# Kernel tuning notes

Measured on AMD Instinct MI355X. Metric: run time of the kernel, lower is better.

The kernel has to match this reference:

```python
import jax, jax.numpy as jnp
import numpy as np

HIDDEN = 1280
HEADS = 16
HEAD_DIM = HIDDEN // HEADS  # 80
B, N = 2, 2048


def _rotate_half(x):
    half = x.shape[-1] // 2
    return jnp.concatenate([-x[..., half:], x[..., :half]], axis=-1)


def setup_inputs() -> dict:
    key = jax.random.key(0)
    ks = jax.random.split(key, 7)
    x = jax.random.normal(ks[0], (B, N, HIDDEN), dtype=jnp.float32)
    cos = jax.random.uniform(ks[1], (N, HEAD_DIM), dtype=jnp.float32)
    sin = jax.random.uniform(ks[2], (N, HEAD_DIM), dtype=jnp.float32)
    s = 1.0 / np.sqrt(HIDDEN)
    qkv_w = jax.random.normal(ks[3], (HIDDEN, 3 * HIDDEN), dtype=jnp.float32) * s
    qkv_b = jax.random.normal(ks[4], (3 * HIDDEN,), dtype=jnp.float32) * 0.02
    proj_w = jax.random.normal(ks[5], (HIDDEN, HIDDEN), dtype=jnp.float32) * s
    proj_b = jax.random.normal(ks[6], (HIDDEN,), dtype=jnp.float32) * 0.02
    return {"x": x, "cos": cos, "sin": sin, "qkv_w": qkv_w, "qkv_b": qkv_b,
            "proj_w": proj_w, "proj_b": proj_b}


def reference(x, cos, sin, qkv_w, qkv_b, proj_w, proj_b):
    b, n, _ = x.shape
    scale = 1.0 / np.sqrt(HEAD_DIM).astype(np.float32)
    # fused QKV projection
    qkv = x @ qkv_w + qkv_b                                # [b, n, 3*hidden]
    qkv = qkv.reshape(b, n, 3, HEADS, HEAD_DIM)
    qkv = jnp.transpose(qkv, (2, 0, 3, 1, 4))              # [3, b, h, n, hd]
    q, k, v = qkv[0], qkv[1], qkv[2]
    # 2D RoPE
    cos_b = cos[None, None, :, :]
    sin_b = sin[None, None, :, :]
    q = q * cos_b + _rotate_half(q) * sin_b
    k = k * cos_b + _rotate_half(k) * sin_b
    # manual softmax attention
    scores = jnp.einsum('bhqd,bhkd->bhqk', q, k) * scale   # [b, h, n, n]
    attn = jax.nn.softmax(scores, axis=-1)
    out = jnp.einsum('bhqk,bhkd->bhqd', attn, v)           # [b, h, n, hd]
    out = jnp.transpose(out, (0, 2, 1, 3)).reshape(b, n, HIDDEN)
    return out @ proj_w + proj_b
```

## Files before the change

kernel.cpp:

```cpp
#include <hip/hip_runtime.h>
#include <hip/hip_bf16.h>
#include <math.h>

#define HIDDEN 1280
#define HEADS 16
#define HD 80
#define HALF 40
#define BB 2
#define NN 2048
#define MROWS (BB * NN)
#define QSCALE ((float)(0.11180339887498949 * 1.4426950408889634))

typedef __attribute__((ext_vector_type(8))) _Float16 f16x8;
typedef __attribute__((ext_vector_type(4))) float f32x4;

#define AS1 __attribute__((address_space(1)))
#define AS3 __attribute__((address_space(3)))

__device__ __forceinline__ void splitf16(float x, ushort& hi, ushort& lo) {
    _Float16 h = (_Float16)x;
    _Float16 l = (_Float16)(x - (float)h);
    hi = __builtin_bit_cast(ushort, h);
    lo = __builtin_bit_cast(ushort, l);
}

__device__ __forceinline__ ushort f2h(float x) {
    _Float16 h = (_Float16)x;
    return __builtin_bit_cast(ushort, h);
}

__device__ __forceinline__ void tsplit_tile(
    const float* __restrict__ W, ushort* __restrict__ T, int K, int N,
    int n0, int k0, float (*s)[33], int tid)
{
    {
        int tn = tid & 31, tk = tid >> 5;
        #pragma unroll
        for (int i = 0; i < 4; ++i)
            s[tk + i * 8][tn] = W[(size_t)(k0 + tk + i * 8) * N + n0 + tn];
    }
    __syncthreads();
    {
        int tk = tid & 31, tn = tid >> 5;
        #pragma unroll
        for (int i = 0; i < 4; ++i)
            T[(size_t)(n0 + tn + i * 8) * K + k0 + tk] = f2h(s[tk][tn + i * 8]);
    }
}

__global__ __launch_bounds__(256) void prep_kernel(
    const float* __restrict__ x, ushort* __restrict__ a_hi,
    ushort* __restrict__ a_lo,
    const float* __restrict__ qkv_w, ushort* __restrict__ wT,
    const float* __restrict__ proj_w, ushort* __restrict__ pT)
{
    __shared__ float s[32][33];
    const int tid = threadIdx.x;
    const int id = blockIdx.x;

    if (id < 5120) {
        int i = id * 256 + tid;
        float4 v = ((const float4*)x)[i];
        ushort4 h, l;
        splitf16(v.x, h.x, l.x);
        splitf16(v.y, h.y, l.y);
        splitf16(v.z, h.z, l.z);
        splitf16(v.w, h.w, l.w);
        ((ushort4*)a_hi)[i] = h;
        ((ushort4*)a_lo)[i] = l;
    } else if (id < 9920) {
        int id2 = id - 5120;
        int n0 = (id2 % 120) * 32, k0 = (id2 / 120) * 32;
        tsplit_tile(qkv_w, wT, HIDDEN, 3 * HIDDEN, n0, k0, s, tid);
    } else {
        int id2 = id - 9920;
        int n0 = (id2 % 40) * 32, k0 = (id2 / 40) * 32;
        tsplit_tile(proj_w, pT, HIDDEN, HIDDEN, n0, k0, s, tid);
    }
}

#define BM 128
#define BN 128
#define BK 32

__global__ __launch_bounds__(256) void gemm_f16x2_kernel(
    const ushort* __restrict__ Ahi, const ushort* __restrict__ Alo,
    const ushort* __restrict__ Bh,
    const float* __restrict__ bias, float* __restrict__ C,
    int M, int N, int K)
{
    __shared__ __align__(16) ushort lds[3 * 128 * 32];

    const int tid = threadIdx.x;
    const int wid = tid >> 6;
    const int lane = tid & 63;
    const int col0 = blockIdx.x * BN;
    const int row0 = blockIdx.y * BM;
    const int wy = wid >> 1, wx = wid & 1;
    const int lrow = lane >> 2;
    const int lchunk = lane & 3;

    f32x4 acc[4][4] = {};

    for (int k0 = 0; k0 < K; k0 += BK) {
        __syncthreads();
        #pragma unroll
        for (int i = 0; i < 6; ++i) {
            int s = wid + i * 4;
            int tile = s >> 3, t = s & 7;
            const ushort* src = (tile == 0) ? Ahi : (tile == 1) ? Alo : Bh;
            int srow = (tile < 2) ? row0 : col0;
            const ushort* g = src + (size_t)(srow + t * 16 + lrow) * K + k0 + lchunk * 8;
            ushort* l = lds + tile * 4096 + t * 512 + lane * 8;
            __builtin_amdgcn_global_load_lds(
                (const AS1 unsigned int*)g, (AS3 unsigned int*)l, 16, 0, 0);
        }
        __syncthreads();

        const int q = lane >> 4;
        const int r = lane & 15;
        f16x8 ah[4], al[4], bf[4];
        #pragma unroll
        for (int i = 0; i < 4; ++i) {
            int arow = wy * 64 + i * 16 + r;
            ah[i] = *(const f16x8*)(lds + 0 * 4096 + arow * 32 + q * 8);
            al[i] = *(const f16x8*)(lds + 1 * 4096 + arow * 32 + q * 8);
            int brow = wx * 64 + i * 16 + r;
            bf[i] = *(const f16x8*)(lds + 2 * 4096 + brow * 32 + q * 8);
        }
        #pragma unroll
        for (int i = 0; i < 4; ++i) {
            #pragma unroll
            for (int j = 0; j < 4; ++j) {
                acc[i][j] = __builtin_amdgcn_mfma_f32_16x16x32_f16(al[i], bf[j], acc[i][j], 0, 0, 0);
                acc[i][j] = __builtin_amdgcn_mfma_f32_16x16x32_f16(ah[i], bf[j], acc[i][j], 0, 0, 0);
            }
        }
    }

    const int q = lane >> 4, r = lane & 15;
    #pragma unroll
    for (int i = 0; i < 4; ++i) {
        #pragma unroll
        for (int j = 0; j < 4; ++j) {
            int col = col0 + wx * 64 + j * 16 + r;
            float b = bias[col];
            #pragma unroll
            for (int v = 0; v < 4; ++v) {
                int row = row0 + wy * 64 + i * 16 + q * 4 + v;
                C[(size_t)row * N + col] = acc[i][j][v] + b;
            }
        }
    }
}

__global__ __launch_bounds__(512, 4) void gemm_f16x2_256x128_kernel(
    const ushort* __restrict__ Ahi, const ushort* __restrict__ Alo,
    const ushort* __restrict__ Bh,
    const float* __restrict__ bias, float* __restrict__ C,
    int M, int N, int K, int nbx)
{
    __shared__ __align__(16) ushort lds[2 * 20480];

    const int tid = threadIdx.x;
    const int wid = tid >> 6;
    const int lane = tid & 63;
    const int q = lane >> 4, r = lane & 15;
    const int wr = wid >> 1;
    const int wc = wid & 1;

    int id = blockIdx.x;
    {
        int nwg = gridDim.x;
        if ((nwg & 7) == 0) {
            int c = nwg >> 3;
            id = (id & 7) * c + (id >> 3);
        }
    }
    const int row0 = (id / nbx) * 256;
    const int col0 = (id % nbx) * 128;

    const ushort* gsrc[5];
    int ldst[5];
    #pragma unroll
    for (int j = 0; j < 5; ++j) {
        if (j < 4) {
            int p = j >> 1;
            int rloc = wid * 32 + (j & 1) * 16 + (lane >> 2);
            int sl = (lane & 3) ^ ((rloc >> 1) & 3);
            const ushort* base = p ? Alo : Ahi;
            gsrc[j] = base + (size_t)(row0 + rloc) * K + sl * 8;
            ldst[j] = p * 8192 + (wid * 32 + (j & 1) * 16) * 32 + lane * 8;
        } else {
            int rloc = wid * 16 + (lane >> 2);
            int sl = (lane & 3) ^ ((rloc >> 1) & 3);
            gsrc[4] = Bh + (size_t)(col0 + rloc) * K + sl * 8;
            ldst[4] = 16384 + wid * 512 + lane * 8;
        }
    }

    const int NT = K / 32;

    #pragma unroll
    for (int j = 0; j < 5; ++j)
        __builtin_amdgcn_global_load_lds((const AS1 unsigned int*)(gsrc[j]),
            (AS3 unsigned int*)(lds + ldst[j]), 16, 0, 0);
    asm volatile("s_waitcnt vmcnt(0)" ::: "memory");
    __builtin_amdgcn_s_barrier();

    const int soff = (q ^ ((r >> 1) & 3)) * 8;
    const int arow0 = wr * 64 + r;
    const int brow0 = wc * 64 + r;

    f32x4 acc[4][4] = {};
    f16x8 ah[4], al[4], bf[2];

    int cb = 0;
    for (int t = 0; t < NT; ++t) {
        const ushort* A0 = lds + cb;
        const ushort* A1 = lds + cb + 8192;
        const ushort* Bp = lds + cb + 16384;
        ushort* nbuf = lds + (20480 - cb);
        const bool st = (t + 1 < NT);
        const int ko = (t + 1) * 32;

        #pragma unroll
        for (int m = 0; m < 4; ++m) {
            int ro = (arow0 + m * 16) * 32 + soff;
            ah[m] = *(const f16x8*)(A0 + ro);
            al[m] = *(const f16x8*)(A1 + ro);
        }
        #pragma unroll
        for (int n = 0; n < 2; ++n)
            bf[n] = *(const f16x8*)(Bp + (brow0 + n * 16) * 32 + soff);
        if (st) {
            __builtin_amdgcn_global_load_lds((const AS1 unsigned int*)(gsrc[0] + ko),
                (AS3 unsigned int*)(nbuf + ldst[0]), 16, 0, 0);
            __builtin_amdgcn_global_load_lds((const AS1 unsigned int*)(gsrc[1] + ko),
                (AS3 unsigned int*)(nbuf + ldst[1]), 16, 0, 0);
            __builtin_amdgcn_global_load_lds((const AS1 unsigned int*)(gsrc[2] + ko),
                (AS3 unsigned int*)(nbuf + ldst[2]), 16, 0, 0);
        }
        __builtin_amdgcn_s_barrier();
        asm volatile("s_waitcnt lgkmcnt(0)" ::: "memory");
        __builtin_amdgcn_sched_barrier(0);
        __builtin_amdgcn_s_setprio(1);
        #pragma unroll
        for (int m = 0; m < 4; ++m) {
            #pragma unroll
            for (int n = 0; n < 2; ++n) {
                acc[m][n] = __builtin_amdgcn_mfma_f32_16x16x32_f16(al[m], bf[n], acc[m][n], 0, 0, 0);
                acc[m][n] = __builtin_amdgcn_mfma_f32_16x16x32_f16(ah[m], bf[n], acc[m][n], 0, 0, 0);
            }
        }
        __builtin_amdgcn_s_setprio(0);
        __builtin_amdgcn_s_barrier();

        #pragma unroll
        for (int n = 0; n < 2; ++n)
            bf[n] = *(const f16x8*)(Bp + (brow0 + (n + 2) * 16) * 32 + soff);
        if (st) {
            __builtin_amdgcn_global_load_lds((const AS1 unsigned int*)(gsrc[3] + ko),
                (AS3 unsigned int*)(nbuf + ldst[3]), 16, 0, 0);
            __builtin_amdgcn_global_load_lds((const AS1 unsigned int*)(gsrc[4] + ko),
                (AS3 unsigned int*)(nbuf + ldst[4]), 16, 0, 0);
        }
        __builtin_amdgcn_s_barrier();
        asm volatile("s_waitcnt lgkmcnt(0)" ::: "memory");
        __builtin_amdgcn_sched_barrier(0);
        __builtin_amdgcn_s_setprio(1);
        #pragma unroll
        for (int m = 0; m < 4; ++m) {
            #pragma unroll
            for (int n = 0; n < 2; ++n) {
                acc[m][n + 2] = __builtin_amdgcn_mfma_f32_16x16x32_f16(al[m], bf[n], acc[m][n + 2], 0, 0, 0);
                acc[m][n + 2] = __builtin_amdgcn_mfma_f32_16x16x32_f16(ah[m], bf[n], acc[m][n + 2], 0, 0, 0);
            }
        }
        __builtin_amdgcn_s_setprio(0);
        asm volatile("s_waitcnt vmcnt(0)" ::: "memory");
        __builtin_amdgcn_s_barrier();
        cb = 20480 - cb;
    }

    #pragma unroll
    for (int m = 0; m < 4; ++m) {
        #pragma unroll
        for (int n = 0; n < 4; ++n) {
            int col = col0 + wc * 64 + n * 16 + r;
            float b = bias[col];
            #pragma unroll
            for (int v = 0; v < 4; ++v) {
                int row = row0 + wr * 64 + m * 16 + q * 4 + v;
                C[(size_t)row * N + col] = acc[m][n][v] + b;
            }
        }
    }
}

__global__ __launch_bounds__(256) void rope_split_kernel(
    const float* __restrict__ qkv, const float* __restrict__ cos_t,
    const float* __restrict__ sin_t,
    ushort* __restrict__ qf, ushort* __restrict__ kf,
    ushort* __restrict__ vt)
{
    __shared__ float s_v[64][84];
    const int tid = threadIdx.x;
    const int b = blockIdx.z, h = blockIdx.y;
    const int n0 = blockIdx.x * 64;
    const int bh = b * HEADS + h;

    #pragma unroll
    for (int i = 0; i < 5; ++i) {
        int u = tid + i * 256;
        int n = u / 20, c = u % 20;
        const float* src = qkv + (size_t)(b * NN + n0 + n) * 3840 + 2 * HIDDEN + h * HD + c * 4;
        *(float4*)(&s_v[n][c * 4]) = *(const float4*)src;
    }

    for (int u = tid; u < 640; u += 256) {
        int n = u / 10, p = u % 10;
        int d = p * 4;
        int ng = n0 + n;
        size_t rowb = (size_t)(b * NN + ng) * 3840;
        float4 c0 = *(const float4*)(cos_t + ng * HD + d);
        float4 c1 = *(const float4*)(cos_t + ng * HD + d + HALF);
        float4 s0 = *(const float4*)(sin_t + ng * HD + d);
        float4 s1 = *(const float4*)(sin_t + ng * HD + d + HALF);
        size_t qo = ((size_t)bh * NN + ng) * 96;
        {
            float4 x0 = *(const float4*)(qkv + rowb + h * HD + d);
            float4 x1 = *(const float4*)(qkv + rowb + h * HD + d + HALF);
            ushort4 h4a, h4b;
            h4a.x = f2h((x0.x * c0.x - x1.x * s0.x) * QSCALE);
            h4a.y = f2h((x0.y * c0.y - x1.y * s0.y) * QSCALE);
            h4a.z = f2h((x0.z * c0.z - x1.z * s0.z) * QSCALE);
            h4a.w = f2h((x0.w * c0.w - x1.w * s0.w) * QSCALE);
            h4b.x = f2h((x1.x * c1.x + x0.x * s1.x) * QSCALE);
            h4b.y = f2h((x1.y * c1.y + x0.y * s1.y) * QSCALE);
            h4b.z = f2h((x1.z * c1.z + x0.z * s1.z) * QSCALE);
            h4b.w = f2h((x1.w * c1.w + x0.w * s1.w) * QSCALE);
            *(ushort4*)(qf + qo + d) = h4a;
            *(ushort4*)(qf + qo + d + HALF) = h4b;
        }
        {
            float4 x0 = *(const float4*)(qkv + rowb + HIDDEN + h * HD + d);
            float4 x1 = *(const float4*)(qkv + rowb + HIDDEN + h * HD + d + HALF);
            ushort4 h4a, h4b;
            h4a.x = f2h(x0.x * c0.x - x1.x * s0.x);
            h4a.y = f2h(x0.y * c0.y - x1.y * s0.y);
            h4a.z = f2h(x0.z * c0.z - x1.z * s0.z);
            h4a.w = f2h(x0.w * c0.w - x1.w * s0.w);
            h4b.x = f2h(x1.x * c1.x + x0.x * s1.x);
            h4b.y = f2h(x1.y * c1.y + x0.y * s1.y);
            h4b.z = f2h(x1.z * c1.z + x0.z * s1.z);
            h4b.w = f2h(x1.w * c1.w + x0.w * s1.w);
            *(ushort4*)(kf + qo + d) = h4a;
            *(ushort4*)(kf + qo + d + HALF) = h4b;
        }
    }

    {
        int which = tid >> 7;
        int u = tid & 127;
        int n = u >> 1, part = u & 1;
        size_t o = ((size_t)bh * NN + n0 + n) * 96 + 80 + part * 8;
        uint4 z = {0u, 0u, 0u, 0u};
        if (which == 0) *(uint4*)(qf + o) = z;
        else            *(uint4*)(kf + o) = z;
    }
    __syncthreads();

    for (int u = tid; u < 320; u += 256) {
        int d = u >> 2, nc = u & 3;
        ushort hs[16];
        #pragma unroll
        for (int kk = 0; kk < 16; ++kk)
            hs[kk] = f2h(s_v[nc * 16 + kk][d]);
        size_t o = ((size_t)bh * HD + d) * NN + n0 + nc * 16;
        uint4 w0, w1;
        w0.x = (uint)hs[0] | ((uint)hs[1] << 16);
        w0.y = (uint)hs[2] | ((uint)hs[3] << 16);
        w0.z = (uint)hs[4] | ((uint)hs[5] << 16);
        w0.w = (uint)hs[6] | ((uint)hs[7] << 16);
        w1.x = (uint)hs[8] | ((uint)hs[9] << 16);
        w1.y = (uint)hs[10] | ((uint)hs[11] << 16);
        w1.z = (uint)hs[12] | ((uint)hs[13] << 16);
        w1.w = (uint)hs[14] | ((uint)hs[15] << 16);
        *(uint4*)(vt + o) = w0;
        *(uint4*)(vt + o + 8) = w1;
    }
}

__global__ __launch_bounds__(512, 4) void attn_mfma_kernel(
    const ushort* __restrict__ qf, const ushort* __restrict__ kf,
    const ushort* __restrict__ vt,
    ushort* __restrict__ ao_hi, ushort* __restrict__ ao_lo)
{
    __shared__ __align__(16) ushort lds[34816];
    _Float16* p_s = (_Float16*)(lds + 26624);

    const int tid = threadIdx.x;
    const int wave = tid >> 6, lane = tid & 63;
    const int quad = lane >> 4, r = lane & 15;
    const int b = blockIdx.z, h = blockIdx.y;
    const int bh = b * HEADS + h;
    const int q0 = blockIdx.x * 128;

    const size_t kb = (size_t)bh * NN * 96;
    const size_t vb = (size_t)bh * HD * NN;

    const ushort* gptr[4];
    int ldso[4];
    #pragma unroll
    for (int i = 0; i < 4; ++i) {
        int s = wave + i * 8;
        if (s < 16) {
            int row = s * 4 + (lane >> 4);
            int t = lane & 15;
            int g = t ^ (row & 7);
            if (g >= 12) g = 0;
            gptr[i] = kf + kb + (size_t)row * 96 + g * 8;
            ldso[i] = s * 512 + lane * 8;
        } else if (s < 26) {
            int ts = s - 16;
            gptr[i] = vt + vb + (size_t)(ts * 8 + (lane >> 3)) * NN
                      + (size_t)(((lane & 7) ^ (lane >> 3)) * 8);
            ldso[i] = 8192 + ts * 512 + lane * 8;
        } else {
            gptr[i] = nullptr;
            ldso[i] = 0;
        }
    }

    f16x8 qfr[3];
    #pragma unroll
    for (int c = 0; c < 3; ++c) {
        size_t o = ((size_t)bh * NN + q0 + wave * 16 + r) * 96 + c * 32 + quad * 8;
        qfr[c] = *(const f16x8*)(qf + o);
    }

    f32x4 oacc[5] = {};
    float l_part[4] = {};

    #pragma unroll
    for (int i = 0; i < 4; ++i) {
        int s = wave + i * 8;
        if (s < 26) {
            __builtin_amdgcn_global_load_lds((const AS1 unsigned int*)gptr[i],
                (AS3 unsigned int*)(lds + ldso[i]), 16, 0, 0);
            gptr[i] += (s < 16) ? 6144 : 64;
        }
    }
    asm volatile("s_waitcnt vmcnt(0)" ::: "memory");
    __builtin_amdgcn_s_barrier();

    int cur = 0;
    for (int j0 = 0; j0 < NN; j0 += 64) {
        const int nxt = 13312 - cur;
        if (j0 + 64 < NN) {
            #pragma unroll
            for (int i = 0; i < 4; ++i) {
                int s = wave + i * 8;
                if (s < 26) {
                    __builtin_amdgcn_global_load_lds((const AS1 unsigned int*)gptr[i],
                        (AS3 unsigned int*)(lds + nxt + ldso[i]), 16, 0, 0);
                    gptr[i] += (s < 16) ? 6144 : 64;
                }
            }
        }

        const ushort* k_s = lds + cur;
        const _Float16* v_s = (const _Float16*)(lds + cur + 8192);

        f32x4 sc[4] = {};
        __builtin_amdgcn_s_setprio(1);
        #pragma unroll
        for (int jt = 0; jt < 4; ++jt) {
            f16x8 kbf[3];
            int j = jt * 16 + r;
            #pragma unroll
            for (int c = 0; c < 3; ++c) {
                int ch = (c * 4 + quad) ^ (r & 7);
                kbf[c] = *(const f16x8*)(k_s + j * 128 + ch * 8);
            }
            #pragma unroll
            for (int c = 0; c < 3; ++c)
                sc[jt] = __builtin_amdgcn_mfma_f32_16x16x32_f16(qfr[c], kbf[c], sc[jt], 0, 0, 0);
        }
        __builtin_amdgcn_s_setprio(0);

        #pragma unroll
        for (int v = 0; v < 4; ++v) {
            float ps = 0.0f;
            #pragma unroll
            for (int jt = 0; jt < 4; ++jt) {
                float p = __builtin_amdgcn_exp2f(sc[jt][v]);
                sc[jt][v] = p;
                ps += p;
            }
            l_part[v] += ps;
        }
        {
            int rowbase = wave * 16 + quad * 4;
            #pragma unroll
            for (int jt = 0; jt < 4; ++jt) {
                int bks = (jt * 2 + (r >> 3)) ^ (quad << 1);
                #pragma unroll
                for (int v = 0; v < 4; ++v)
                    p_s[(rowbase + v) * 64 + bks * 8 + (r & 7)] = (_Float16)sc[jt][v];
            }
        }

        f16x8 pa[2];
        #pragma unroll
        for (int cc = 0; cc < 2; ++cc) {
            int rowp = wave * 16 + r;
            int bks = (cc * 4 + quad) ^ (((r >> 2) & 3) << 1);
            pa[cc] = *(const f16x8*)(p_s + rowp * 64 + bks * 8);
        }

        __builtin_amdgcn_s_setprio(1);
        #pragma unroll
        for (int dt = 0; dt < 5; ++dt)
            #pragma unroll
            for (int cc = 0; cc < 2; ++cc) {
                int ck = (cc * 4 + quad) ^ (r & 7);
                f16x8 vbf = *(const f16x8*)(v_s + (dt * 16 + r) * 64 + ck * 8);
                oacc[dt] = __builtin_amdgcn_mfma_f32_16x16x32_f16(pa[cc], vbf, oacc[dt], 0, 0, 0);
            }
        __builtin_amdgcn_s_setprio(0);

        asm volatile("s_waitcnt vmcnt(0)" ::: "memory");
        __builtin_amdgcn_s_barrier();
        cur = nxt;
    }

    float inv_l[4];
    #pragma unroll
    for (int v = 0; v < 4; ++v) {
        float l = l_part[v];
        l += __shfl_xor(l, 1);
        l += __shfl_xor(l, 2);
        l += __shfl_xor(l, 4);
        l += __shfl_xor(l, 8);
        inv_l[v] = 1.0f / l;
    }

    __syncthreads();
    #pragma unroll
    for (int v = 0; v < 4; ++v) {
        int row = wave * 16 + quad * 4 + v;
        #pragma unroll
        for (int dt = 0; dt < 5; ++dt) {
            float o = oacc[dt][v] * inv_l[v];
            ushort hh, ll;
            splitf16(o, hh, ll);
            lds[row * 80 + dt * 16 + r] = hh;
            lds[10240 + row * 80 + dt * 16 + r] = ll;
        }
    }
    __syncthreads();
    {
        size_t gbase = ((size_t)b * NN + q0) * HIDDEN + h * HD;
        #pragma unroll
        for (int i = 0; i < 5; ++i) {
            int u = tid + i * 512;
            int plane = u / 1280, idx = u % 1280;
            int row = idx / 10, part = idx % 10;
            uint4 w = *(const uint4*)(lds + plane * 10240 + idx * 8);
            ushort* dst = (plane ? ao_lo : ao_hi) + gbase + (size_t)row * HIDDEN + part * 8;
            *(uint4*)dst = w;
        }
    }
}

extern "C" void kernel_launch(void* const* d_in, const int* in_sizes, int n_in,
                              void* d_out, int out_size, void* d_ws, size_t ws_size,
                              hipStream_t stream)
{
    const float* x      = (const float*)d_in[0];
    const float* cos_t  = (const float*)d_in[1];
    const float* sin_t  = (const float*)d_in[2];
    const float* qkv_w  = (const float*)d_in[3];
    const float* qkv_b  = (const float*)d_in[4];
    const float* proj_w = (const float*)d_in[5];
    const float* proj_b = (const float*)d_in[6];
    float* out = (float*)d_out;

    char* ws = (char*)d_ws;
    float*  qkv   = (float*)ws;
    ushort* ao_hi = (ushort*)ws;
    ushort* ao_lo = (ushort*)(ws + 10485760);
    ushort* wT    = (ushort*)(ws + 62914560);
    ushort* vt    = (ushort*)(ws + 62914560);
    ushort* a_hi  = (ushort*)(ws + 82575360);
    ushort* a_lo  = (ushort*)(ws + 93061120);
    ushort* q_f   = (ushort*)(ws + 83886080);
    ushort* k_f   = (ushort*)(ws + 96468992);
    ushort* pT    = (ushort*)(ws + 109051904);

    prep_kernel<<<dim3(11520), 256, 0, stream>>>(
        x, a_hi, a_lo, qkv_w, wT, proj_w, pT);

    gemm_f16x2_256x128_kernel<<<dim3((MROWS / 256) * (3 * HIDDEN / 128)), 512, 0, stream>>>(
        a_hi, a_lo, wT, qkv_b, qkv, MROWS, 3 * HIDDEN, HIDDEN, 3 * HIDDEN / 128);

    rope_split_kernel<<<dim3(NN / 64, HEADS, BB), 256, 0, stream>>>(
        qkv, cos_t, sin_t, q_f, k_f, vt);

    attn_mfma_kernel<<<dim3(NN / 128, HEADS, BB), 512, 0, stream>>>(
        q_f, k_f, vt, ao_hi, ao_lo);

    gemm_f16x2_kernel<<<dim3(HIDDEN / BN, MROWS / BM), 256, 0, stream>>>(
        ao_hi, ao_lo, pT, proj_b, out, MROWS, HIDDEN, HIDDEN);
}
```

Measured before the change: 315.8 us.

## Double-buffer 128x128 GEMM and simplify 256x128 GEMM pipeline to single phase

The 128x128 split-f16 GEMM moves from a load-then-compute loop with two syncthreads per step to a double-buffered LDS scheme. The next K tile is prefetched with global_load_lds while MFMAs run on the current buffer, which is meant to hide global-load latency. The 256x128 kernel drops its two-phase interleaving, where loads were split around half the MFMAs with extra barriers. It now issues all prefetches up front and runs all 16 MFMA pairs in one block, which means fewer barriers but more live fragment registers and possibly less fine-grained overlap.

```diff
diff --git a/kernel.cpp b/kernel.cpp
--- a/kernel.cpp
+++ b/kernel.cpp
@@ -89,7 +89,7 @@
     const float* __restrict__ bias, float* __restrict__ C,
     int M, int N, int K)
 {
-    __shared__ __align__(16) ushort lds[3 * 128 * 32];
+    __shared__ __align__(16) ushort lds[2 * 12288];
 
     const int tid = threadIdx.x;
     const int wid = tid >> 6;
@@ -99,34 +99,52 @@
     const int wy = wid >> 1, wx = wid & 1;
     const int lrow = lane >> 2;
     const int lchunk = lane & 3;
+    const int q = lane >> 4;
+    const int r = lane & 15;
+
+    const ushort* gsrc[6];
+    int ldst[6];
+    #pragma unroll
+    for (int i = 0; i < 6; ++i) {
+        int s = wid + i * 4;
+        int tile = s >> 3, t = s & 7;
+        const ushort* src = (tile == 0) ? Ahi : (tile == 1) ? Alo : Bh;
+        int srow = (tile < 2) ? row0 : col0;
+        gsrc[i] = src + (size_t)(srow + t * 16 + lrow) * K + lchunk * 8;
+        ldst[i] = tile * 4096 + t * 512 + lane * 8;
+    }
+
+    const int NT = K / BK;
+
+    #pragma unroll
+    for (int i = 0; i < 6; ++i)
+        __builtin_amdgcn_global_load_lds((const AS1 unsigned int*)(gsrc[i]),
+            (AS3 unsigned int*)(lds + ldst[i]), 16, 0, 0);
+    asm volatile("s_waitcnt vmcnt(0)" ::: "memory");
+    __builtin_amdgcn_s_barrier();
 
     f32x4 acc[4][4] = {};
-
-    for (int k0 = 0; k0 < K; k0 += BK) {
-        __syncthreads();
-        #pragma unroll
-        for (int i = 0; i < 6; ++i) {
-            int s = wid + i * 4;
-            int tile = s >> 3, t = s & 7;
-            const ushort* src = (tile == 0) ? Ahi : (tile == 1) ? Alo : Bh;
-            int srow = (tile < 2) ? row0 : col0;
-            const ushort* g = src + (size_t)(srow + t * 16 + lrow) * K + k0 + lchunk * 8;
-            ushort* l = lds + tile * 4096 + t * 512 + lane * 8;
-            __builtin_amdgcn_global_load_lds(
-                (const AS1 unsigned int*)g, (AS3 unsigned int*)l, 16, 0, 0);
-        }
-        __syncthreads();
-
-        const int q = lane >> 4;
-        const int r = lane & 15;
+    int cb = 0;
+
+    for (int t = 0; t < NT; ++t) {
+        const ushort* base = lds + cb;
+        ushort* nbuf = lds + (12288 - cb);
+        if (t + 1 < NT) {
+            const int ko = (t + 1) * BK;
+            #pragma unroll
+            for (int i = 0; i < 6; ++i)
+                __builtin_amdgcn_global_load_lds((const AS1 unsigned int*)(gsrc[i] + ko),
+                    (AS3 unsigned int*)(nbuf + ldst[i]), 16, 0, 0);
+        }
+
         f16x8 ah[4], al[4], bf[4];
         #pragma unroll
         for (int i = 0; i < 4; ++i) {
             int arow = wy * 64 + i * 16 + r;
-            ah[i] = *(const f16x8*)(lds + 0 * 4096 + arow * 32 + q * 8);
-            al[i] = *(const f16x8*)(lds + 1 * 4096 + arow * 32 + q * 8);
+            ah[i] = *(const f16x8*)(base + 0 * 4096 + arow * 32 + q * 8);
+            al[i] = *(const f16x8*)(base + 1 * 4096 + arow * 32 + q * 8);
             int brow = wx * 64 + i * 16 + r;
-            bf[i] = *(const f16x8*)(lds + 2 * 4096 + brow * 32 + q * 8);
+            bf[i] = *(const f16x8*)(base + 2 * 4096 + brow * 32 + q * 8);
         }
         #pragma unroll
         for (int i = 0; i < 4; ++i) {
@@ -136,9 +154,12 @@
                 acc[i][j] = __builtin_amdgcn_mfma_f32_16x16x32_f16(ah[i], bf[j], acc[i][j], 0, 0, 0);
             }
         }
-    }
-
-    const int q = lane >> 4, r = lane & 15;
+
+        asm volatile("s_waitcnt vmcnt(0)" ::: "memory");
+        __builtin_amdgcn_s_barrier();
+        cb = 12288 - cb;
+    }
+
     #pragma unroll
     for (int i = 0; i < 4; ++i) {
         #pragma unroll
@@ -213,7 +234,6 @@
     const int brow0 = wc * 64 + r;
 
     f32x4 acc[4][4] = {};
-    f16x8 ah[4], al[4], bf[2];
 
     int cb = 0;
     for (int t = 0; t < NT; ++t) {
@@ -221,9 +241,16 @@
         const ushort* A1 = lds + cb + 8192;
         const ushort* Bp = lds + cb + 16384;
         ushort* nbuf = lds + (20480 - cb);
-        const bool st = (t + 1 < NT);
-        const int ko = (t + 1) * 32;
-
+
+        if (t + 1 < NT) {
+            const int ko = (t + 1) * 32;
+            #pragma unroll
+            for (int j = 0; j < 5; ++j)
+                __builtin_amdgcn_global_load_lds((const AS1 unsigned int*)(gsrc[j] + ko),
+                    (AS3 unsigned int*)(nbuf + ldst[j]), 16, 0, 0);
+        }
+
+        f16x8 ah[4], al[4], bf[4];
         #pragma unroll
         for (int m = 0; m < 4; ++m) {
             int ro = (arow0 + m * 16) * 32 + soff;
@@ -231,53 +258,20 @@
             al[m] = *(const f16x8*)(A1 + ro);
         }
         #pragma unroll
-        for (int n = 0; n < 2; ++n)
+        for (int n = 0; n < 4; ++n)
             bf[n] = *(const f16x8*)(Bp + (brow0 + n * 16) * 32 + soff);
-        if (st) {
-            __builtin_amdgcn_global_load_lds((const AS1 unsigned int*)(gsrc[0] + ko),
-                (AS3 unsigned int*)(nbuf + ldst[0]), 16, 0, 0);
-            __builtin_amdgcn_global_load_lds((const AS1 unsigned int*)(gsrc[1] + ko),
-                (AS3 unsigned int*)(nbuf + ldst[1]), 16, 0, 0);
-            __builtin_amdgcn_global_load_lds((const AS1 unsigned int*)(gsrc[2] + ko),
-                (AS3 unsigned int*)(nbuf + ldst[2]), 16, 0, 0);
-        }
-        __builtin_amdgcn_s_barrier();
-        asm volatile("s_waitcnt lgkmcnt(0)" ::: "memory");
-        __builtin_amdgcn_sched_barrier(0);
+
         __builtin_amdgcn_s_setprio(1);
         #pragma unroll
         for (int m = 0; m < 4; ++m) {
             #pragma unroll
-            for (int n = 0; n < 2; ++n) {
+            for (int n = 0; n < 4; ++n) {
                 acc[m][n] = __builtin_amdgcn_mfma_f32_16x16x32_f16(al[m], bf[n], acc[m][n], 0, 0, 0);
                 acc[m][n] = __builtin_amdgcn_mfma_f32_16x16x32_f16(ah[m], bf[n], acc[m][n], 0, 0, 0);
             }
         }
         __builtin_amdgcn_s_setprio(0);
-        __builtin_amdgcn_s_barrier();
-
-        #pragma unroll
-        for (int n = 0; n < 2; ++n)
-            bf[n] = *(const f16x8*)(Bp + (brow0 + (n + 2) * 16) * 32 + soff);
-        if (st) {
-            __builtin_amdgcn_global_load_lds((const AS1 unsigned int*)(gsrc[3] + ko),
-                (AS3 unsigned int*)(nbuf + ldst[3]), 16, 0, 0);
-            __builtin_amdgcn_global_load_lds((const AS1 unsigned int*)(gsrc[4] + ko),
-                (AS3 unsigned int*)(nbuf + ldst[4]), 16, 0, 0);
-        }
-        __builtin_amdgcn_s_barrier();
-        asm volatile("s_waitcnt lgkmcnt(0)" ::: "memory");
-        __builtin_amdgcn_sched_barrier(0);
-        __builtin_amdgcn_s_setprio(1);
-        #pragma unroll
-        for (int m = 0; m < 4; ++m) {
-            #pragma unroll
-            for (int n = 0; n < 2; ++n) {
-                acc[m][n + 2] = __builtin_amdgcn_mfma_f32_16x16x32_f16(al[m], bf[n], acc[m][n + 2], 0, 0, 0);
-                acc[m][n + 2] = __builtin_amdgcn_mfma_f32_16x16x32_f16(ah[m], bf[n], acc[m][n + 2], 0, 0, 0);
-            }
-        }
-        __builtin_amdgcn_s_setprio(0);
+
         asm volatile("s_waitcnt vmcnt(0)" ::: "memory");
         __builtin_amdgcn_s_barrier();
         cb = 20480 - cb;
```

Result: no change. 316.0 us (+0.1%).

## Double-buffer LDS tiles in 128x128 f16x2 GEMM to overlap loads with MFMA

Applied to the files above, without the earlier changes.

Doubles the LDS staging buffer in the 128x128 GEMM kernel and prefetches the next K-tile with global_load_lds while MFMAs consume the current one. Per-thread source and destination addresses are precomputed, and the two __syncthreads per iteration become one waitcnt plus barrier. The aim is to hide global-load latency behind compute. In exchange LDS use per block doubles to 48 KB, which may lower occupancy. Which GEMMs use this kernel rather than the 256x128 variant is not visible.

```diff
diff --git a/kernel.cpp b/kernel.cpp
--- a/kernel.cpp
+++ b/kernel.cpp
@@ -89,7 +89,7 @@
     const float* __restrict__ bias, float* __restrict__ C,
     int M, int N, int K)
 {
-    __shared__ __align__(16) ushort lds[3 * 128 * 32];
+    __shared__ __align__(16) ushort lds[2 * 12288];
 
     const int tid = threadIdx.x;
     const int wid = tid >> 6;
@@ -99,34 +99,52 @@
     const int wy = wid >> 1, wx = wid & 1;
     const int lrow = lane >> 2;
     const int lchunk = lane & 3;
+    const int q = lane >> 4;
+    const int r = lane & 15;
+
+    const ushort* gsrc[6];
+    int ldst[6];
+    #pragma unroll
+    for (int i = 0; i < 6; ++i) {
+        int s = wid + i * 4;
+        int tile = s >> 3, t = s & 7;
+        const ushort* src = (tile == 0) ? Ahi : (tile == 1) ? Alo : Bh;
+        int srow = (tile < 2) ? row0 : col0;
+        gsrc[i] = src + (size_t)(srow + t * 16 + lrow) * K + lchunk * 8;
+        ldst[i] = tile * 4096 + t * 512 + lane * 8;
+    }
+
+    const int NT = K / BK;
+
+    #pragma unroll
+    for (int i = 0; i < 6; ++i)
+        __builtin_amdgcn_global_load_lds((const AS1 unsigned int*)(gsrc[i]),
+            (AS3 unsigned int*)(lds + ldst[i]), 16, 0, 0);
+    asm volatile("s_waitcnt vmcnt(0)" ::: "memory");
+    __builtin_amdgcn_s_barrier();
 
     f32x4 acc[4][4] = {};
-
-    for (int k0 = 0; k0 < K; k0 += BK) {
-        __syncthreads();
-        #pragma unroll
-        for (int i = 0; i < 6; ++i) {
-            int s = wid + i * 4;
-            int tile = s >> 3, t = s & 7;
-            const ushort* src = (tile == 0) ? Ahi : (tile == 1) ? Alo : Bh;
-            int srow = (tile < 2) ? row0 : col0;
-            const ushort* g = src + (size_t)(srow + t * 16 + lrow) * K + k0 + lchunk * 8;
-            ushort* l = lds + tile * 4096 + t * 512 + lane * 8;
-            __builtin_amdgcn_global_load_lds(
-                (const AS1 unsigned int*)g, (AS3 unsigned int*)l, 16, 0, 0);
-        }
-        __syncthreads();
-
-        const int q = lane >> 4;
-        const int r = lane & 15;
+    int cb = 0;
+
+    for (int t = 0; t < NT; ++t) {
+        const ushort* base = lds + cb;
+        ushort* nbuf = lds + (12288 - cb);
+        if (t + 1 < NT) {
+            const int ko = (t + 1) * BK;
+            #pragma unroll
+            for (int i = 0; i < 6; ++i)
+                __builtin_amdgcn_global_load_lds((const AS1 unsigned int*)(gsrc[i] + ko),
+                    (AS3 unsigned int*)(nbuf + ldst[i]), 16, 0, 0);
+        }
+
         f16x8 ah[4], al[4], bf[4];
         #pragma unroll
         for (int i = 0; i < 4; ++i) {
             int arow = wy * 64 + i * 16 + r;
-            ah[i] = *(const f16x8*)(lds + 0 * 4096 + arow * 32 + q * 8);
-            al[i] = *(const f16x8*)(lds + 1 * 4096 + arow * 32 + q * 8);
+            ah[i] = *(const f16x8*)(base + 0 * 4096 + arow * 32 + q * 8);
+            al[i] = *(const f16x8*)(base + 1 * 4096 + arow * 32 + q * 8);
             int brow = wx * 64 + i * 16 + r;
-            bf[i] = *(const f16x8*)(lds + 2 * 4096 + brow * 32 + q * 8);
+            bf[i] = *(const f16x8*)(base + 2 * 4096 + brow * 32 + q * 8);
         }
         #pragma unroll
         for (int i = 0; i < 4; ++i) {
@@ -136,9 +154,12 @@
                 acc[i][j] = __builtin_amdgcn_mfma_f32_16x16x32_f16(ah[i], bf[j], acc[i][j], 0, 0, 0);
             }
         }
-    }
-
-    const int q = lane >> 4, r = lane & 15;
+
+        asm volatile("s_waitcnt vmcnt(0)" ::: "memory");
+        __builtin_amdgcn_s_barrier();
+        cb = 12288 - cb;
+    }
+
     #pragma unroll
     for (int i = 0; i < 4; ++i) {
         #pragma unroll
```

New measurement: 306.1 us. -3.1%, faster.
